# Optimization experiments

Hardware: AMD Instinct MI355X
Metric: run time of the kernel (lower is better)

## Reference

```python
import jax, jax.numpy as jnp
import numpy as np

# norse LIFParameters defaults
TAU_MEM_INV = 100.0
V_TH = 1.0
V_LEAK = 0.0
V_RESET = 0.0
ALPHA = 100.0  # superspike surrogate slope
DT = 0.001
SEQ_LENGTH = 100


@jax.custom_vjp
def heaviside(x):
    return (x > 0).astype(x.dtype)


def _heaviside_fwd(x):
    return heaviside(x), x


def _heaviside_bwd(x, g):
    # norse 'super' method: superspike surrogate gradient 1/(alpha*|x|+1)^2
    return (g / (ALPHA * jnp.abs(x) + 1.0) ** 2,)


heaviside.defvjp(_heaviside_fwd, _heaviside_bwd)


def setup_inputs() -> dict:
    key = jax.random.key(0)
    # positive input currents in [0, 2): values > ~1 cross threshold at some latency
    input_current = jax.random.uniform(key, (256, 4096), dtype=jnp.float32) * 2.0
    return {"input_current": input_current}


def reference(input_current):
    def step(carry, _):
        v, mask = carry
        # lif_current_encoder: dv = dt * tau_mem_inv * ((v_leak - v) + I)
        v = v + DT * TAU_MEM_INV * ((V_LEAK - v) + input_current)
        z = heaviside(v - V_TH)
        v = v - z * (v - V_RESET)
        # latency encoding: suppress any spike after the first one
        spike = jnp.where(mask > 0, jnp.zeros_like(z), z)
        return (v, mask + z), spike

    init = (jnp.zeros_like(input_current), jnp.zeros_like(input_current))
    _, spikes = jax.lax.scan(step, init, None, length=SEQ_LENGTH)
    return spikes  # [seq_length, *input_current.shape]
```

## Files before the change

### kernel.cpp

```cpp
#include <hip/hip_runtime.h>


#define SEQ_LEN 100

__global__ __launch_bounds__(256) void lif_latency_kernel(
    const float4* __restrict__ in, float4* __restrict__ out, int n4) {
    int i = blockIdx.x * blockDim.x + threadIdx.x;
    if (i >= n4) return;

    float4 I4 = in[i];
    float Iv[4] = {I4.x, I4.y, I4.z, I4.w};
    int ts[4];

    #pragma unroll
    for (int c = 0; c < 4; ++c) {
        float Ic = Iv[c];
        float v = 0.0f;
        int t = 0;
        for (; t < SEQ_LEN; ++t) {
            float d = __fadd_rn(__fsub_rn(0.0f, v), Ic);
            v = __fadd_rn(v, __fmul_rn(0.1f, d));
            if (v > 1.0f) break;
        }
        ts[c] = t;
    }

    float4* o = out + i;
    #pragma unroll 4
    for (int t = 0; t < SEQ_LEN; ++t) {
        float4 val;
        val.x = (t == ts[0]) ? 1.0f : 0.0f;
        val.y = (t == ts[1]) ? 1.0f : 0.0f;
        val.z = (t == ts[2]) ? 1.0f : 0.0f;
        val.w = (t == ts[3]) ? 1.0f : 0.0f;
        o[(size_t)t * n4] = val;
    }
}

extern "C" void kernel_launch(void* const* d_in, const int* in_sizes, int n_in,
                              void* d_out, int out_size, void* d_ws, size_t ws_size,
                              hipStream_t stream) {
    const float* in = (const float*)d_in[0];
    float* out = (float*)d_out;
    int n = in_sizes[0];
    int n4 = n / 4;
    int threads = 256;
    int blocks = (n4 + threads - 1) / threads;
    lif_latency_kernel<<<blocks, threads, 0, stream>>>(
        (const float4*)in, (float4*)out, n4);
}
```

Before: 441.4 us.

## Split LIF into spike-time kernel and massively parallel nontemporal store kernel

Splits the work into two kernels. The first computes each neuron's first-spike time and writes it as a byte to workspace. The second launches a 2D grid over neurons and timesteps, so each thread writes one float4 with a nontemporal store. This exposes far more parallelism for the 420MB output write than the original 1024 blocks each looping over 100 strided stores. In exchange it adds a second launch and a small workspace round trip, and the store kernel has no bounds check, so it assumes n4 is a multiple of 256.

```diff
diff --git a/kernel.cpp b/kernel.cpp
--- a/kernel.cpp
+++ b/kernel.cpp
@@ -3,14 +3,16 @@
 
 #define SEQ_LEN 100
 
-__global__ __launch_bounds__(256) void lif_latency_kernel(
-    const float4* __restrict__ in, float4* __restrict__ out, int n4) {
+typedef float nfloat4 __attribute__((ext_vector_type(4)));
+
+__global__ __launch_bounds__(256) void lif_compute_ts(
+    const float4* __restrict__ in, uchar4* __restrict__ ts_out, int n4) {
     int i = blockIdx.x * blockDim.x + threadIdx.x;
     if (i >= n4) return;
 
     float4 I4 = in[i];
     float Iv[4] = {I4.x, I4.y, I4.z, I4.w};
-    int ts[4];
+    unsigned char ts[4];
 
     #pragma unroll
     for (int c = 0; c < 4; ++c) {
@@ -22,30 +24,42 @@
             v = __fadd_rn(v, __fmul_rn(0.1f, d));
             if (v > 1.0f) break;
         }
-        ts[c] = t;
+        ts[c] = (unsigned char)t;
     }
+    ts_out[i] = make_uchar4(ts[0], ts[1], ts[2], ts[3]);
+}
 
-    float4* o = out + i;
-    #pragma unroll 4
-    for (int t = 0; t < SEQ_LEN; ++t) {
-        float4 val;
-        val.x = (t == ts[0]) ? 1.0f : 0.0f;
-        val.y = (t == ts[1]) ? 1.0f : 0.0f;
-        val.z = (t == ts[2]) ? 1.0f : 0.0f;
-        val.w = (t == ts[3]) ? 1.0f : 0.0f;
-        o[(size_t)t * n4] = val;
-    }
+__global__ __launch_bounds__(256) void lif_store_spikes(
+    const uchar4* __restrict__ ts_in, nfloat4* __restrict__ out, int n4) {
+    int i = blockIdx.x * blockDim.x + threadIdx.x;
+    int t = blockIdx.y;
+    uchar4 ts = ts_in[i];
+
+    nfloat4 val;
+    val.x = (ts.x == (unsigned char)t) ? 1.0f : 0.0f;
+    val.y = (ts.y == (unsigned char)t) ? 1.0f : 0.0f;
+    val.z = (ts.z == (unsigned char)t) ? 1.0f : 0.0f;
+    val.w = (ts.w == (unsigned char)t) ? 1.0f : 0.0f;
+
+    __builtin_nontemporal_store(val, &out[(size_t)t * n4 + i]);
 }
 
 extern "C" void kernel_launch(void* const* d_in, const int* in_sizes, int n_in,
                               void* d_out, int out_size, void* d_ws, size_t ws_size,
                               hipStream_t stream) {
     const float* in = (const float*)d_in[0];
-    float* out = (float*)d_out;
     int n = in_sizes[0];
     int n4 = n / 4;
+
+    uchar4* ts_buf = (uchar4*)d_ws;
+
     int threads = 256;
-    int blocks = (n4 + threads - 1) / threads;
-    lif_latency_kernel<<<blocks, threads, 0, stream>>>(
-        (const float4*)in, (float4*)out, n4);
+    int blocks_x = (n4 + threads - 1) / threads;
+
+    lif_compute_ts<<<blocks_x, threads, 0, stream>>>(
+        (const float4*)in, ts_buf, n4);
+
+    dim3 grid(blocks_x, SEQ_LEN);
+    lif_store_spikes<<<grid, threads, 0, stream>>>(
+        (const uchar4*)ts_buf, (nfloat4*)d_out, n4);
 }
```

After: 452.3 us. 1.02x slower.
